# Optimization experiments

Measured on AMD Instinct MI355X. Metric: run time of the kernel, lower is better.

Reference implementation:

```python
import jax, jax.numpy as jnp
import numpy as np

H = 16  # number of heads

def setup_inputs() -> dict:
    key = jax.random.key(0)
    ks = jax.random.split(key, 8)
    B, T, D = 4, 2048, 1024
    s = 0.02
    return {
        "query": jax.random.normal(ks[0], (B, T, D), jnp.float32),
        "key":   jax.random.normal(ks[1], (B, T, D), jnp.float32),
        "value": jax.random.normal(ks[2], (B, T, D), jnp.float32),
        "mask":  jnp.ones((B, T, T), jnp.int32),
        # torch nn.Linear weights: [out_features, in_features]
        "Wq": jax.random.normal(ks[3], (D, D), jnp.float32) * s,
        "Wk": jax.random.normal(ks[4], (D, D), jnp.float32) * s,
        "Wv": jax.random.normal(ks[5], (D, D), jnp.float32) * s,
        "Wo": jax.random.normal(ks[6], (D, D), jnp.float32) * s,
        "bo": jnp.zeros((D,), jnp.float32),
    }

def reference(query, key, value, mask, Wq, Wk, Wv, Wo, bo):
    B, Tq, _ = query.shape
    Tk = key.shape[1]
    Dv = Wv.shape[0]
    # linear projections (y = x @ W^T), split into heads: [B, H, T, dh]
    Q = jnp.einsum('btd,ed->bte', query, Wq).reshape(B, Tq, H, -1).transpose(0, 2, 1, 3)
    K = jnp.einsum('btd,ed->bte', key,   Wk).reshape(B, Tk, H, -1).transpose(0, 2, 1, 3)
    V = jnp.einsum('btd,ed->bte', value, Wv).reshape(B, Tk, H, -1).transpose(0, 2, 1, 3)
    d_k = K.shape[-1]
    scores = jnp.einsum('bhqd,bhkd->bhqk', Q, K) / jnp.sqrt(jnp.asarray(d_k, Q.dtype))
    # mask broadcast: [B,1,Tq,Tk]; masked_fill(mask==0, -1e9)
    scores = jnp.where(mask[:, None] == 0, jnp.asarray(-1e9, scores.dtype), scores)
    attn = jax.nn.softmax(scores, axis=-1)
    Z = jnp.einsum('bhqk,bhkd->bhqd', attn, V)          # [B,H,Tq,dh]
    Zc = Z.transpose(0, 2, 1, 3).reshape(B, Tq, Dv)     # concat heads
    return jnp.einsum('btd,ed->bte', Zc, Wo) + bo
```

## Files before the change

### kernel.cpp

```cpp
#include <hip/hip_runtime.h>

typedef __bf16 bf16x8 __attribute__((ext_vector_type(8)));
typedef float f32x4 __attribute__((ext_vector_type(4)));
typedef unsigned short u16;
typedef unsigned long long u64;

#define NX 8388608
#define NW 1048576

__device__ __forceinline__ u16 f2bf(float f) {
  union { float f; unsigned u; } c; c.f = f;
  unsigned u = c.u;
  u += 0x7fffu + ((u >> 16) & 1u);
  return (u16)(u >> 16);
}

__device__ __forceinline__ f32x4 mfma16(bf16x8 a, bf16x8 b, f32x4 c) {
  return __builtin_amdgcn_mfma_f32_16x16x32_bf16(a, b, c, 0, 0, 0);
}

__device__ __forceinline__ void gld16(void* lds, const void* g) {
  __builtin_amdgcn_global_load_lds(
      (const __attribute__((address_space(1))) unsigned int*)g,
      (__attribute__((address_space(3))) unsigned int*)lds, 16, 0, 0);
}

__global__ __launch_bounds__(256) void cast_all(
    const float* __restrict__ q, const float* __restrict__ k,
    const float* __restrict__ v, const float* __restrict__ wq,
    const float* __restrict__ wk, const float* __restrict__ wv,
    const float* __restrict__ wo, u16* __restrict__ xbf, u16* __restrict__ wbf) {
  long long i = ((long long)blockIdx.x * 256 + threadIdx.x) * 8;
  const float* src; u16* dst; long long off;
  if (i < (long long)NX)            { src = q; dst = xbf;            off = i; }
  else if (i < 2LL * NX)            { src = k; dst = xbf + NX;       off = i - NX; }
  else if (i < 3LL * NX)            { src = v; dst = xbf + 2LL * NX; off = i - 2LL * NX; }
  else {
    long long j = i - 3LL * NX;
    int w = (int)(j / NW); off = j - (long long)w * NW;
    src = (w == 0) ? wq : (w == 1) ? wk : (w == 2) ? wv : wo;
    dst = wbf + (long long)w * NW;
  }
  float4 a = *(const float4*)(src + off);
  float4 b = *(const float4*)(src + off + 4);
  u16 o[8] = {f2bf(a.x), f2bf(a.y), f2bf(a.z), f2bf(a.w),
              f2bf(b.x), f2bf(b.y), f2bf(b.z), f2bf(b.w)};
  *(uint4*)(dst + off) = *(const uint4*)o;
}

__global__ __launch_bounds__(256) void mask_pack(
    const int* __restrict__ mask, u64* __restrict__ bits) {
  const int row = blockIdx.x * 4 + (threadIdx.x >> 6);
  const int lane = threadIdx.x & 63;
  const int* mrow = mask + (long long)row * 2048;
#pragma unroll
  for (int it = 0; it < 32; it++) {
    u64 w = __ballot(mrow[it * 64 + lane] != 0);
    if (lane == 0) bits[row * 32 + it] = w;
  }
}

template <int MODE>
__global__ __launch_bounds__(256, 2) void gemm128(
    const u16* __restrict__ Abase, const u16* __restrict__ Wbase,
    u16* __restrict__ oq, u16* __restrict__ ok, u16* __restrict__ ovt,
    const float* __restrict__ bias, float* __restrict__ of) {
  __shared__ u16 smem[2][128 * 64];
  u16* sA = smem[0];
  u16* sB = smem[1];
  const u16* A = Abase;
  const u16* W = Wbase;
  if (MODE == 0) { A += (long long)blockIdx.z * NX; W += (long long)blockIdx.z * NW; }
  const int tid = threadIdx.x, wave = tid >> 6, lane = tid & 63;
  const int quad = lane >> 4, l15 = lane & 15;
  const int m0 = blockIdx.y * 128, n0 = blockIdx.x * 128;
  const int wm = (wave & 1) * 64, wn = (wave >> 1) * 64;
  const int lr = lane >> 3;
  const int gc = (lane & 7) ^ lr;
  f32x4 acc[4][4];
#pragma unroll
  for (int i = 0; i < 4; i++)
#pragma unroll
    for (int j = 0; j < 4; j++) acc[i][j] = (f32x4){0.f, 0.f, 0.f, 0.f};

  for (int ks = 0; ks < 16; ks++) {
    const int k0 = ks * 64;
    __syncthreads();
#pragma unroll
    for (int t = 0; t < 4; t++) {
      const int rb = wave * 32 + t * 8;
      gld16(&sA[rb * 64], &A[(m0 + rb + lr) * 1024 + k0 + gc * 8]);
      gld16(&sB[rb * 64], &W[(n0 + rb + lr) * 1024 + k0 + gc * 8]);
    }
    __syncthreads();
#pragma unroll
    for (int kc = 0; kc < 2; kc++) {
      bf16x8 aF[4], bF[4];
#pragma unroll
      for (int i = 0; i < 4; i++)
        aF[i] = *(const bf16x8*)&sA[(wm + 16 * i + l15) * 64 +
                                    (((kc * 4 + quad) ^ (l15 & 7)) * 8)];
#pragma unroll
      for (int j = 0; j < 4; j++)
        bF[j] = *(const bf16x8*)&sB[(wn + 16 * j + l15) * 64 +
                                    (((kc * 4 + quad) ^ (l15 & 7)) * 8)];
#pragma unroll
      for (int i = 0; i < 4; i++)
#pragma unroll
        for (int j = 0; j < 4; j++) acc[i][j] = mfma16(aF[i], bF[j], acc[i][j]);
    }
  }

  if (MODE == 0) {
    const int z = blockIdx.z;
    if (z < 2) {
      u16* dst = (z == 0) ? oq : ok;
#pragma unroll
      for (int i = 0; i < 4; i++)
#pragma unroll
        for (int j = 0; j < 4; j++)
#pragma unroll
          for (int r = 0; r < 4; r++) {
            int m = m0 + wm + 16 * i + quad * 4 + r;
            int n = n0 + wn + 16 * j + l15;
            int b = m >> 11, t = m & 2047, h = n >> 6, d = n & 63;
            dst[(((b << 4) + h) * 2048 + t) * 64 + d] = f2bf(acc[i][j][r]);
          }
    } else {
      __syncthreads();
      u16* sT = &smem[0][0] + wave * 4096;
#pragma unroll
      for (int i = 0; i < 4; i++)
#pragma unroll
        for (int j = 0; j < 4; j++)
#pragma unroll
          for (int r = 0; r < 4; r++) {
            int m = 16 * i + quad * 4 + r;
            int n = 16 * j + l15;
            sT[n * 64 + (((m >> 3) ^ (n & 7)) * 8) + (m & 7)] = f2bf(acc[i][j][r]);
          }
      const int b = m0 >> 11, t0 = (m0 + wm) & 2047;
      const int h = (n0 + wn) >> 6;
      u16* dst = ovt + ((long long)((b << 4) + h)) * 131072 + lane * 2048 + t0;
#pragma unroll
      for (int c = 0; c < 8; c++) {
        uint4 val = *(const uint4*)&sT[lane * 64 + ((c ^ (lane & 7)) * 8)];
        *(uint4*)(dst + c * 8) = val;
      }
    }
  } else {
    float bb[4];
#pragma unroll
    for (int j = 0; j < 4; j++) bb[j] = bias[n0 + wn + 16 * j + l15];
#pragma unroll
    for (int i = 0; i < 4; i++)
#pragma unroll
      for (int j = 0; j < 4; j++)
#pragma unroll
        for (int r = 0; r < 4; r++) {
          int m = m0 + wm + 16 * i + quad * 4 + r;
          int n = n0 + wn + 16 * j + l15;
          of[m * 1024 + n] = acc[i][j][r] + bb[j];
        }
  }
}

__global__ __launch_bounds__(256, 3) void attn(
    const u16* __restrict__ Qh, const u16* __restrict__ Kh,
    const u16* __restrict__ Vt, const u64* __restrict__ mbits,
    u16* __restrict__ Zc) {
  __shared__ u16 sK[128 * 64];
  __shared__ u16 sV[64 * 128];
  __shared__ __bf16 sP[4][16][136];
  const int tid = threadIdx.x, wave = tid >> 6, lane = tid & 63;
  const int quad = lane >> 4, l15 = lane & 15;
  const int bh = blockIdx.y, b = bh >> 4, h = bh & 15, qt = blockIdx.x;
  const int q0 = qt * 64 + wave * 16;
  const int lr8 = lane >> 3, gc8 = (lane & 7) ^ (lr8 & 7);
  const int lr4 = lane >> 4, lc16 = lane & 15;

  bf16x8 qa[2];
#pragma unroll
  for (int kc = 0; kc < 2; kc++)
    qa[kc] = *(const bf16x8*)&Qh[(bh * 2048 + q0 + l15) * 64 + kc * 32 + quad * 8];

  const u64* mb = mbits + (long long)(b * 2048 + q0 + quad * 4) * 32;

  f32x4 oacc[4];
#pragma unroll
  for (int j = 0; j < 4; j++) oacc[j] = (f32x4){0.f, 0.f, 0.f, 0.f};
  float lv[4] = {0.f, 0.f, 0.f, 0.f};
  const float cexp = 0.18033688f;

  for (int kt = 0; kt < 16; kt++) {
    __syncthreads();
#pragma unroll
    for (int t = 0; t < 4; t++) {
      const int rbk = wave * 32 + t * 8;
      gld16(&sK[rbk * 64], &Kh[(bh * 2048 + kt * 128 + rbk + lr8) * 64 + gc8 * 8]);
      const int rbv = wave * 16 + t * 4;
      gld16(&sV[rbv * 128],
            &Vt[(bh * 64 + rbv + lr4) * 2048 + kt * 128 + ((lc16 ^ (t * 4 + lr4)) * 8)]);
    }
    u64 mw[4][2];
#pragma unroll
    for (int r = 0; r < 4; r++) {
      mw[r][0] = mb[r * 32 + 2 * kt];
      mw[r][1] = mb[r * 32 + 2 * kt + 1];
    }
    __syncthreads();

    f32x4 sacc[8];
#pragma unroll
    for (int j = 0; j < 8; j++) sacc[j] = (f32x4){0.f, 0.f, 0.f, 0.f};
#pragma unroll
    for (int kc = 0; kc < 2; kc++)
#pragma unroll
      for (int j = 0; j < 8; j++) {
        bf16x8 kF = *(const bf16x8*)&sK[(16 * j + l15) * 64 +
                                        (((kc * 4 + quad) ^ (l15 & 7)) * 8)];
        sacc[j] = mfma16(qa[kc], kF, sacc[j]);
      }

    bool full = __all((mw[0][0] & mw[0][1] & mw[1][0] & mw[1][1] &
                       mw[2][0] & mw[2][1] & mw[3][0] & mw[3][1]) == ~0ull);
    if (full) {
#pragma unroll
      for (int j = 0; j < 8; j++)
#pragma unroll
        for (int r = 0; r < 4; r++) {
          float p = exp2f(sacc[j][r] * cexp);
          lv[r] += p;
          sP[wave][quad * 4 + r][16 * j + l15] = (__bf16)p;
        }
    } else {
#pragma unroll
      for (int j = 0; j < 8; j++)
#pragma unroll
        for (int r = 0; r < 4; r++) {
          u64 w = mw[r][j >> 2];
          float p = ((w >> (16 * (j & 3) + l15)) & 1ull)
                        ? exp2f(sacc[j][r] * cexp) : 0.f;
          lv[r] += p;
          sP[wave][quad * 4 + r][16 * j + l15] = (__bf16)p;
        }
    }

#pragma unroll
    for (int kc = 0; kc < 4; kc++) {
      bf16x8 aP = *(const bf16x8*)&sP[wave][l15][kc * 32 + quad * 8];
#pragma unroll
      for (int j = 0; j < 4; j++) {
        bf16x8 vF = *(const bf16x8*)&sV[(16 * j + l15) * 128 +
                                        (((kc * 4 + quad) ^ l15) * 8)];
        oacc[j] = mfma16(aP, vF, oacc[j]);
      }
    }
  }

  float inv[4];
#pragma unroll
  for (int r = 0; r < 4; r++) {
    float s = lv[r];
    s += __shfl_xor(s, 1);
    s += __shfl_xor(s, 2);
    s += __shfl_xor(s, 4);
    s += __shfl_xor(s, 8);
    inv[r] = 1.f / s;
  }
#pragma unroll
  for (int j = 0; j < 4; j++)
#pragma unroll
    for (int r = 0; r < 4; r++) {
      int t = q0 + quad * 4 + r;
      Zc[(b * 2048 + t) * 1024 + h * 64 + 16 * j + l15] = f2bf(oacc[j][r] * inv[r]);
    }
}

extern "C" void kernel_launch(void* const* d_in, const int* in_sizes, int n_in,
                              void* d_out, int out_size, void* d_ws, size_t ws_size,
                              hipStream_t stream) {
  (void)in_sizes; (void)n_in; (void)out_size; (void)ws_size;
  const float* q    = (const float*)d_in[0];
  const float* k    = (const float*)d_in[1];
  const float* v    = (const float*)d_in[2];
  const int*   mask = (const int*)d_in[3];
  const float* Wq   = (const float*)d_in[4];
  const float* Wk   = (const float*)d_in[5];
  const float* Wv   = (const float*)d_in[6];
  const float* Wo   = (const float*)d_in[7];
  const float* bo   = (const float*)d_in[8];
  float* out = (float*)d_out;

  u16* Xbf = (u16*)d_ws;
  u16* Wbf = Xbf + 3LL * NX;
  u16* Qh  = Wbf + 4LL * NW;
  u16* Kh  = Qh + (long long)NX;
  u16* Vt  = Kh + (long long)NX;
  u16* Zc  = Vt + (long long)NX;
  u64* Mb  = (u64*)(Zc + (long long)NX);

  cast_all<<<14336, 256, 0, stream>>>(q, k, v, Wq, Wk, Wv, Wo, Xbf, Wbf);
  mask_pack<<<2048, 256, 0, stream>>>(mask, Mb);
  gemm128<0><<<dim3(8, 64, 3), 256, 0, stream>>>(Xbf, Wbf, Qh, Kh, Vt, nullptr, nullptr);
  attn<<<dim3(32, 64), 256, 0, stream>>>(Qh, Kh, Vt, Mb, Zc);
  gemm128<1><<<dim3(8, 64), 256, 0, stream>>>(Zc, Wbf + 3LL * NW, nullptr, nullptr, nullptr,
                                              bo, out);
}
```

Baseline: 457.1 us.

## Fold softmax scale into Q projection and permute K rows for vectorized P stores

Multiplies Q by the softmax exp2 scale in the projection epilogue, so the attention kernel calls the raw hardware exp2 without a per-element multiply. K rows are loaded into shared memory in a permuted order, so each lane's 8 score columns become contiguous keys. That lets each row of P be packed into one 16-byte vector store instead of scalar bf16 stores. Mask bit extraction is rewritten to match the permuted key order; the permutation has to stay consistent with the P·V operand layout, and the raw exp2 builtin may give up some accuracy.

```diff
diff --git a/kernel.cpp b/kernel.cpp
--- a/kernel.cpp
+++ b/kernel.cpp
@@ -114,6 +114,7 @@
   if (MODE == 0) {
     const int z = blockIdx.z;
     if (z < 2) {
+      const float qscale = (z == 0) ? 0.18033688f : 1.0f;
       u16* dst = (z == 0) ? oq : ok;
 #pragma unroll
       for (int i = 0; i < 4; i++)
@@ -124,7 +125,7 @@
             int m = m0 + wm + 16 * i + quad * 4 + r;
             int n = n0 + wn + 16 * j + l15;
             int b = m >> 11, t = m & 2047, h = n >> 6, d = n & 63;
-            dst[(((b << 4) + h) * 2048 + t) * 64 + d] = f2bf(acc[i][j][r]);
+            dst[(((b << 4) + h) * 2048 + t) * 64 + d] = f2bf(acc[i][j][r] * qscale);
           }
     } else {
       __syncthreads();
@@ -171,7 +172,7 @@
     u16* __restrict__ Zc) {
   __shared__ u16 sK[128 * 64];
   __shared__ u16 sV[64 * 128];
-  __shared__ __bf16 sP[4][16][136];
+  __shared__ alignas(16) u16 sP[4][16][136];
   const int tid = threadIdx.x, wave = tid >> 6, lane = tid & 63;
   const int quad = lane >> 4, l15 = lane & 15;
   const int bh = blockIdx.y, b = bh >> 4, h = bh & 15, qt = blockIdx.x;
@@ -190,14 +191,14 @@
 #pragma unroll
   for (int j = 0; j < 4; j++) oacc[j] = (f32x4){0.f, 0.f, 0.f, 0.f};
   float lv[4] = {0.f, 0.f, 0.f, 0.f};
-  const float cexp = 0.18033688f;
 
   for (int kt = 0; kt < 16; kt++) {
     __syncthreads();
 #pragma unroll
     for (int t = 0; t < 4; t++) {
       const int rbk = wave * 32 + t * 8;
-      gld16(&sK[rbk * 64], &Kh[(bh * 2048 + kt * 128 + rbk + lr8) * 64 + gc8 * 8]);
+      const int kap = (((rbk & 15) + lr8) << 3) + (rbk >> 4);
+      gld16(&sK[rbk * 64], &Kh[(bh * 2048 + kt * 128 + kap) * 64 + gc8 * 8]);
       const int rbv = wave * 16 + t * 4;
       gld16(&sV[rbv * 128],
             &Vt[(bh * 64 + rbv + lr4) * 2048 + kt * 128 + ((lc16 ^ (t * 4 + lr4)) * 8)]);
@@ -226,24 +227,34 @@
                        mw[2][0] & mw[2][1] & mw[3][0] & mw[3][1]) == ~0ull);
     if (full) {
 #pragma unroll
-      for (int j = 0; j < 8; j++)
-#pragma unroll
-        for (int r = 0; r < 4; r++) {
-          float p = exp2f(sacc[j][r] * cexp);
-          lv[r] += p;
-          sP[wave][quad * 4 + r][16 * j + l15] = (__bf16)p;
+      for (int r = 0; r < 4; r++) {
+        bf16x8 pk;
+        float ls = 0.f;
+#pragma unroll
+        for (int j = 0; j < 8; j++) {
+          float p = __builtin_amdgcn_exp2f(sacc[j][r]);
+          ls += p;
+          pk[j] = (__bf16)p;
         }
+        lv[r] += ls;
+        *(bf16x8*)&sP[wave][quad * 4 + r][l15 * 8] = pk;
+      }
     } else {
 #pragma unroll
-      for (int j = 0; j < 8; j++)
-#pragma unroll
-        for (int r = 0; r < 4; r++) {
-          u64 w = mw[r][j >> 2];
-          float p = ((w >> (16 * (j & 3) + l15)) & 1ull)
-                        ? exp2f(sacc[j][r] * cexp) : 0.f;
-          lv[r] += p;
-          sP[wave][quad * 4 + r][16 * j + l15] = (__bf16)p;
+      for (int r = 0; r < 4; r++) {
+        bf16x8 pk;
+        float ls = 0.f;
+        u64 w = mw[r][l15 >> 3];
+#pragma unroll
+        for (int j = 0; j < 8; j++) {
+          float p = __builtin_amdgcn_exp2f(sacc[j][r]);
+          p = ((w >> (((l15 & 7) << 3) + j)) & 1ull) ? p : 0.f;
+          ls += p;
+          pk[j] = (__bf16)p;
         }
+        lv[r] += ls;
+        *(bf16x8*)&sP[wave][quad * 4 + r][l15 * 8] = pk;
+      }
     }
 
 #pragma unroll
```

After: 400.2 us. 12.4% less time.
